# Performance work log

Hardware: AMD Instinct MI355X
Metric: run time of the kernel (lower is better)

## Reference

```python
import jax, jax.numpy as jnp
import numpy as np

B, S, H, NH = 4, 2048, 1024, 16
HD = H // NH  # head dim 64


def setup_inputs() -> dict:
    key = jax.random.key(0)
    ks = jax.random.split(key, 8)
    s = 1.0 / np.sqrt(H)
    return {
        "hidden_states": jax.random.normal(ks[0], (B, S, H), dtype=jnp.float32),
        "attention_mask": jnp.zeros((B, 1, 1, S), dtype=jnp.float32),
        "Wq": jax.random.normal(ks[1], (H, H), dtype=jnp.float32) * s,
        "bq": jnp.zeros((H,), dtype=jnp.float32),
        "Wk": jax.random.normal(ks[2], (H, H), dtype=jnp.float32) * s,
        "bk": jnp.zeros((H,), dtype=jnp.float32),
        "Wv": jax.random.normal(ks[3], (H, H), dtype=jnp.float32) * s,
        "bv": jnp.zeros((H,), dtype=jnp.float32),
    }


def _split_heads(x):
    # [B,S,H] -> [B,NH,S,HD]
    b, s, _ = x.shape
    return x.reshape(b, s, NH, HD).transpose(0, 2, 1, 3)


def reference(hidden_states, attention_mask, Wq, bq, Wk, bk, Wv, bv):
    q = _split_heads(hidden_states @ Wq.T + bq)
    k = _split_heads(hidden_states @ Wk.T + bk)
    v = _split_heads(hidden_states @ Wv.T + bv)

    qk = jnp.einsum("bhid,bhjd->bhij", q, k)  # [B,NH,S,S]
    seq = q.shape[2]
    causal = jnp.triu(jnp.ones((seq, seq), dtype=bool), 1)  # True above diagonal
    attn_w = jnp.where(causal, -jnp.inf, qk) + attention_mask
    # NOTE: original divides by sqrt(d_k) AFTER masking/adding attention_mask
    probs = jax.nn.softmax(attn_w / jnp.sqrt(jnp.float32(HD)), axis=-1)
    out = jnp.einsum("bhij,bhjd->bhid", probs, v)  # [B,NH,S,HD]
    return out.transpose(0, 2, 1, 3).reshape(hidden_states.shape[0], seq, NH * HD)
```

## Files before the change

### kernel.cpp

```cpp
#include <hip/hip_runtime.h>


#define B_   4
#define S_   2048
#define H_   1024
#define NH_  16
#define HD_  64
#define M_   (B_ * S_)

#define CEXP 0.18033688011112042f

#define SWZ(row, col) ((col) ^ (((row) & 7) << 3))

typedef float          f32x4  __attribute__((ext_vector_type(4)));
typedef short          bf16x8 __attribute__((ext_vector_type(8)));
typedef unsigned short u16x8  __attribute__((ext_vector_type(8)));
typedef unsigned int   u32x2  __attribute__((ext_vector_type(2)));

__device__ __forceinline__ unsigned short f2bf(float f) {
    unsigned int u = __float_as_uint(f);
    u += 0x7fffu + ((u >> 16) & 1u);
    return (unsigned short)(u >> 16);
}

__device__ __forceinline__ unsigned int cvt_pk_bf16(float lo, float hi) {
    unsigned int r;
    asm("v_cvt_pk_bf16_f32 %0, %1, %2" : "=v"(r) : "v"(lo), "v"(hi));
    return r;
}

__device__ __forceinline__ void load16_lds(const unsigned short* g, unsigned short* l) {
    __builtin_amdgcn_global_load_lds(
        (const __attribute__((address_space(1))) unsigned int*)g,
        (__attribute__((address_space(3))) unsigned int*)l, 16, 0, 0);
}

__global__ __launch_bounds__(256) void cast_bf16(
    const float* __restrict__ s0, const float* __restrict__ s1,
    const float* __restrict__ s2, const float* __restrict__ s3,
    const float* __restrict__ s4,
    unsigned short* __restrict__ d0, unsigned short* __restrict__ d1,
    unsigned short* __restrict__ d2, unsigned short* __restrict__ d3,
    float* __restrict__ d4) {
    const int bid = blockIdx.x;
    if (bid >= 5632) {
        int i = ((bid - 5632) * 256 + (int)threadIdx.x) * 8;
        if (i + 8 <= B_ * S_) {
            float4 a = *(const float4*)(s4 + i);
            float4 b = *(const float4*)(s4 + i + 4);
            a.x *= CEXP; a.y *= CEXP; a.z *= CEXP; a.w *= CEXP;
            b.x *= CEXP; b.y *= CEXP; b.z *= CEXP; b.w *= CEXP;
            *(float4*)(d4 + i)     = a;
            *(float4*)(d4 + i + 4) = b;
        }
        return;
    }
    const float* src;
    unsigned short* dst;
    int base;
    if (bid < 4096)      { src = s0; dst = d0; base = bid; }
    else if (bid < 4608) { src = s1; dst = d1; base = bid - 4096; }
    else if (bid < 5120) { src = s2; dst = d2; base = bid - 4608; }
    else                 { src = s3; dst = d3; base = bid - 5120; }
    int i = (base * 256 + (int)threadIdx.x) * 8;
    float4 a = *(const float4*)(src + i);
    float4 b = *(const float4*)(src + i + 4);
    u16x8 o;
    o[0] = f2bf(a.x); o[1] = f2bf(a.y); o[2] = f2bf(a.z); o[3] = f2bf(a.w);
    o[4] = f2bf(b.x); o[5] = f2bf(b.y); o[6] = f2bf(b.z); o[7] = f2bf(b.w);
    *(u16x8*)(dst + i) = o;
}

__global__ __launch_bounds__(256, 3) void qkv_gemm(
    const unsigned short* __restrict__ A,
    const unsigned short* __restrict__ W0, const unsigned short* __restrict__ W1,
    const unsigned short* __restrict__ W2,
    const float* __restrict__ b0, const float* __restrict__ b1,
    const float* __restrict__ b2,
    unsigned short* __restrict__ o0, unsigned short* __restrict__ o1,
    unsigned short* __restrict__ o2) {
    __shared__ unsigned short smem[2 * 128 * 64];
    unsigned short* sA = smem;
    unsigned short* sB = smem + 128 * 64;
    unsigned short* sT = smem;

    const int t = threadIdx.x;
    const int w = t >> 6, lane = t & 63, quad = lane >> 4, l15 = lane & 15;
    const int bm = blockIdx.x, bn = blockIdx.y, z = blockIdx.z;

    const unsigned short* W = (z == 0) ? W0 : (z == 1) ? W1 : W2;
    const float*        bia = (z == 0) ? b0 : (z == 1) ? b1 : b2;

    const int wm = (w & 1) * 64, wn = (w >> 1) * 64;

    f32x4 acc[4][4];
#pragma unroll
    for (int i = 0; i < 4; ++i)
#pragma unroll
        for (int j = 0; j < 4; ++j) acc[i][j] = f32x4{0.f, 0.f, 0.f, 0.f};

    const int srow = w * 32 + (lane >> 3);
    const int scol = (lane & 7) * 8;
    const unsigned short* Ag = A + (size_t)(bm * 128 + srow) * H_ + scol;
    const unsigned short* Wg = W + (size_t)(bn * 128 + srow) * H_ + scol;
    unsigned short* lA = &sA[w * 32 * 64];
    unsigned short* lB = &sB[w * 32 * 64];

    for (int kt = 0; kt < 16; ++kt) {
        __syncthreads();
#pragma unroll
        for (int c = 0; c < 4; ++c) {
            load16_lds(Ag + kt * 64 + (size_t)c * 8 * H_, lA + c * 512);
            load16_lds(Wg + kt * 64 + (size_t)c * 8 * H_, lB + c * 512);
        }
        __syncthreads();
#pragma unroll
        for (int kk = 0; kk < 64; kk += 32) {
            bf16x8 af[4], bf[4];
#pragma unroll
            for (int mi = 0; mi < 4; ++mi)
                af[mi] = *(const bf16x8*)&sA[(wm + mi * 16 + l15) * 64 + kk + quad * 8];
#pragma unroll
            for (int ni = 0; ni < 4; ++ni)
                bf[ni] = *(const bf16x8*)&sB[(wn + ni * 16 + l15) * 64 + kk + quad * 8];
#pragma unroll
            for (int mi = 0; mi < 4; ++mi)
#pragma unroll
                for (int ni = 0; ni < 4; ++ni)
                    acc[mi][ni] = __builtin_amdgcn_mfma_f32_16x16x32_bf16(
                        af[mi], bf[ni], acc[mi][ni], 0, 0, 0);
        }
    }

    float bvv[4];
#pragma unroll
    for (int ni = 0; ni < 4; ++ni) bvv[ni] = bia[bn * 128 + wn + ni * 16 + l15];

    if (z != 2) {
        unsigned short* outp = (z == 0) ? o0 : o1;
#pragma unroll
        for (int mi = 0; mi < 4; ++mi)
#pragma unroll
            for (int ni = 0; ni < 4; ++ni)
#pragma unroll
                for (int r = 0; r < 4; ++r) {
                    int m = bm * 128 + wm + mi * 16 + quad * 4 + r;
                    int n = bn * 128 + wn + ni * 16 + l15;
                    outp[(size_t)m * H_ + n] = f2bf(acc[mi][ni][r] + bvv[ni]);
                }
    } else {
        __syncthreads();
        const int halfw = w >> 1;
        const int bb = bm >> 4;
        const int s0 = (bm * 128) & 2047;
        for (int half = 0; half < 2; ++half) {
            if (half) __syncthreads();
            if (halfw == half) {
#pragma unroll
                for (int mi = 0; mi < 4; ++mi)
#pragma unroll
                    for (int ni = 0; ni < 4; ++ni)
#pragma unroll
                        for (int r = 0; r < 4; ++r) {
                            int nl = ni * 16 + l15;
                            int m  = wm + mi * 16 + quad * 4 + r;
                            sT[nl * 136 + m] = f2bf(acc[mi][ni][r] + bvv[ni]);
                        }
            }
            __syncthreads();
            {
                int nl = t >> 2, mc = (t & 3) * 32;
                int ng = bn * 128 + half * 64 + nl;
                int hh = ng >> 6, d = ng & 63;
                size_t base = ((size_t)((bb * NH_ + hh) * HD_ + d)) * S_ + s0 + mc;
#pragma unroll
                for (int i = 0; i < 4; ++i)
                    *(u16x8*)(o2 + base + i * 8) = *(const u16x8*)&sT[nl * 136 + mc + i * 8];
            }
        }
    }
}

__global__ __launch_bounds__(256, 3) void attn(
    const unsigned short* __restrict__ qg, const unsigned short* __restrict__ kg,
    const unsigned short* __restrict__ vtg, const float* __restrict__ mcg,
    float* __restrict__ outg) {
    __shared__ unsigned short k_s[2][64 * 64];
    __shared__ unsigned short v_s[2][64 * 64];
    __shared__ unsigned short p_s[4][16 * 64];

    const int t = threadIdx.x;
    const int w = t >> 6, lane = t & 63, quad = lane >> 4, l15 = lane & 15;
    const int lid = blockIdx.x;
    const int bh = (lid & 7) + ((lid >> 7) << 3);
    const int qt = (lid >> 3) & 15;
    const int b = bh >> 4, h = bh & 15;
    const int qa = qt, qb = 31 - qt;

    const int rs_ = t >> 2;
    const int cs_ = (t & 3) * 16;
    const int sc0 = rs_ * 64 + SWZ(rs_, cs_);
    const int sc1 = rs_ * 64 + SWZ(rs_, cs_ + 8);

    const unsigned short* kbase = kg + ((size_t)b * S_ + rs_) * H_ + h * HD_ + cs_;
    const unsigned short* vbase = vtg + ((size_t)bh * HD_ + rs_) * S_ + cs_;
    const float* mrow = mcg + b * S_ + quad * 4;

    bf16x8 aqa[2], aqb[2];
    {
        const unsigned short* qpa =
            qg + ((size_t)(b * S_ + qa * 64 + w * 16 + l15)) * H_ + h * HD_ + quad * 8;
        aqa[0] = *(const bf16x8*)qpa;
        aqa[1] = *(const bf16x8*)(qpa + 32);
        const unsigned short* qpb =
            qg + ((size_t)(b * S_ + qb * 64 + w * 16 + l15)) * H_ + h * HD_ + quad * 8;
        aqb[0] = *(const bf16x8*)qpb;
        aqb[1] = *(const bf16x8*)(qpb + 32);
    }

    u16x8 pk0 = *(const u16x8*)kbase, pk1 = *(const u16x8*)(kbase + 8);
    u16x8 pv0 = *(const u16x8*)vbase, pv1 = *(const u16x8*)(vbase + 8);

    f32x4 oa[4], ob[4];
    float lsa = 0.f, lsb = 0.f;
#pragma unroll
    for (int dt = 0; dt < 4; ++dt) {
        oa[dt] = f32x4{0.f, 0.f, 0.f, 0.f};
        ob[dt] = f32x4{0.f, 0.f, 0.f, 0.f};
    }

    const int iga0  = qa * 64 + w * 16 + quad * 4;
    const int igb0  = qb * 64 + w * 16 + quad * 4;
    const int qcola = qa * 64 + w * 16 + l15;
    const int qcolb = qb * 64 + w * 16 + l15;
    const int pwr0 = l15 * 64;

    for (int kt = 0; kt <= qb; ++kt) {
        const int cur = kt & 1;
        *(u16x8*)&k_s[cur][sc0] = pk0;
        *(u16x8*)&k_s[cur][sc1] = pk1;
        *(u16x8*)&v_s[cur][sc0] = pv0;
        *(u16x8*)&v_s[cur][sc1] = pv1;
        if (kt < qb) {
            const unsigned short* kp = kbase + (size_t)(kt + 1) * 64 * H_;
            pk0 = *(const u16x8*)kp; pk1 = *(const u16x8*)(kp + 8);
            const unsigned short* vp = vbase + (kt + 1) * 64;
            pv0 = *(const u16x8*)vp; pv1 = *(const u16x8*)(vp + 8);
        }
        __syncthreads();

        float4 mcv[4];
#pragma unroll
        for (int jt = 0; jt < 4; ++jt)
            mcv[jt] = *(const float4*)(mrow + kt * 64 + jt * 16);

        {
            f32x4 sc[4];
#pragma unroll
            for (int jt = 0; jt < 4; ++jt) sc[jt] = f32x4{0.f, 0.f, 0.f, 0.f};
            __builtin_amdgcn_s_setprio(1);
#pragma unroll
            for (int c = 0; c < 2; ++c)
#pragma unroll
                for (int jt = 0; jt < 4; ++jt) {
                    int row = jt * 16 + l15;
                    bf16x8 bk = *(const bf16x8*)&k_s[cur][row * 64 + SWZ(row, c * 32 + quad * 8)];
                    sc[jt] = __builtin_amdgcn_mfma_f32_16x16x32_bf16(bk, aqb[c], sc[jt], 0, 0, 0);
                }
            __builtin_amdgcn_s_setprio(0);
            const bool diag = (kt == qb);
#pragma unroll
            for (int jt = 0; jt < 4; ++jt) {
                const int sb0 = kt * 64 + jt * 16 + quad * 4;
                float p0 = __builtin_amdgcn_exp2f(__builtin_fmaf(sc[jt][0], CEXP, mcv[jt].x));
                float p1 = __builtin_amdgcn_exp2f(__builtin_fmaf(sc[jt][1], CEXP, mcv[jt].y));
                float p2 = __builtin_amdgcn_exp2f(__builtin_fmaf(sc[jt][2], CEXP, mcv[jt].z));
                float p3 = __builtin_amdgcn_exp2f(__builtin_fmaf(sc[jt][3], CEXP, mcv[jt].w));
                if (diag) {
                    if (sb0 + 0 > qcolb) p0 = 0.f;
                    if (sb0 + 1 > qcolb) p1 = 0.f;
                    if (sb0 + 2 > qcolb) p2 = 0.f;
                    if (sb0 + 3 > qcolb) p3 = 0.f;
                }
                lsb += (p0 + p1) + (p2 + p3);
                u32x2 pw;
                pw[0] = cvt_pk_bf16(p0, p1);
                pw[1] = cvt_pk_bf16(p2, p3);
                *(u32x2*)&p_s[w][pwr0 + SWZ(l15, jt * 16 + quad * 4)] = pw;
            }
            __builtin_amdgcn_s_setprio(1);
#pragma unroll
            for (int c = 0; c < 2; ++c) {
                bf16x8 ap = *(const bf16x8*)&p_s[w][l15 * 64 + SWZ(l15, c * 32 + quad * 8)];
#pragma unroll
                for (int dt = 0; dt < 4; ++dt) {
                    int row = dt * 16 + l15;
                    bf16x8 bv = *(const bf16x8*)&v_s[cur][row * 64 + SWZ(row, c * 32 + quad * 8)];
                    ob[dt] = __builtin_amdgcn_mfma_f32_16x16x32_bf16(ap, bv, ob[dt], 0, 0, 0);
                }
            }
            __builtin_amdgcn_s_setprio(0);
        }
        if (kt <= qa) {
            f32x4 sc[4];
#pragma unroll
            for (int jt = 0; jt < 4; ++jt) sc[jt] = f32x4{0.f, 0.f, 0.f, 0.f};
            __builtin_amdgcn_s_setprio(1);
#pragma unroll
            for (int c = 0; c < 2; ++c)
#pragma unroll
                for (int jt = 0; jt < 4; ++jt) {
                    int row = jt * 16 + l15;
                    bf16x8 bk = *(const bf16x8*)&k_s[cur][row * 64 + SWZ(row, c * 32 + quad * 8)];
                    sc[jt] = __builtin_amdgcn_mfma_f32_16x16x32_bf16(bk, aqa[c], sc[jt], 0, 0, 0);
                }
            __builtin_amdgcn_s_setprio(0);
            const bool diag = (kt == qa);
#pragma unroll
            for (int jt = 0; jt < 4; ++jt) {
                const int sb0 = kt * 64 + jt * 16 + quad * 4;
                float p0 = __builtin_amdgcn_exp2f(__builtin_fmaf(sc[jt][0], CEXP, mcv[jt].x));
                float p1 = __builtin_amdgcn_exp2f(__builtin_fmaf(sc[jt][1], CEXP, mcv[jt].y));
                float p2 = __builtin_amdgcn_exp2f(__builtin_fmaf(sc[jt][2], CEXP, mcv[jt].z));
                float p3 = __builtin_amdgcn_exp2f(__builtin_fmaf(sc[jt][3], CEXP, mcv[jt].w));
                if (diag) {
                    if (sb0 + 0 > qcola) p0 = 0.f;
                    if (sb0 + 1 > qcola) p1 = 0.f;
                    if (sb0 + 2 > qcola) p2 = 0.f;
                    if (sb0 + 3 > qcola) p3 = 0.f;
                }
                lsa += (p0 + p1) + (p2 + p3);
                u32x2 pw;
                pw[0] = cvt_pk_bf16(p0, p1);
                pw[1] = cvt_pk_bf16(p2, p3);
                *(u32x2*)&p_s[w][pwr0 + SWZ(l15, jt * 16 + quad * 4)] = pw;
            }
            __builtin_amdgcn_s_setprio(1);
#pragma unroll
            for (int c = 0; c < 2; ++c) {
                bf16x8 ap = *(const bf16x8*)&p_s[w][l15 * 64 + SWZ(l15, c * 32 + quad * 8)];
#pragma unroll
                for (int dt = 0; dt < 4; ++dt) {
                    int row = dt * 16 + l15;
                    bf16x8 bv = *(const bf16x8*)&v_s[cur][row * 64 + SWZ(row, c * 32 + quad * 8)];
                    oa[dt] = __builtin_amdgcn_mfma_f32_16x16x32_bf16(ap, bv, oa[dt], 0, 0, 0);
                }
            }
            __builtin_amdgcn_s_setprio(0);
        }
    }

    float sa = lsa, sb = lsb;
    sa += __shfl_xor(sa, 16); sa += __shfl_xor(sa, 32);
    sb += __shfl_xor(sb, 16); sb += __shfl_xor(sb, 32);
    float ra[4], rb[4];
#pragma unroll
    for (int r = 0; r < 4; ++r) {
        int src = (quad << 4) | (quad * 4 + r);
        ra[r] = 1.0f / __shfl(sa, src);
        rb[r] = 1.0f / __shfl(sb, src);
    }
#pragma unroll
    for (int dt = 0; dt < 4; ++dt)
#pragma unroll
        for (int r = 0; r < 4; ++r) {
            int col = h * HD_ + dt * 16 + l15;
            outg[(size_t)(b * S_ + iga0 + r) * H_ + col] = oa[dt][r] * ra[r];
            outg[(size_t)(b * S_ + igb0 + r) * H_ + col] = ob[dt][r] * rb[r];
        }
}

extern "C" void kernel_launch(void* const* d_in, const int* in_sizes, int n_in,
                              void* d_out, int out_size, void* d_ws, size_t ws_size,
                              hipStream_t stream) {
    const float* hs   = (const float*)d_in[0];
    const float* mask = (const float*)d_in[1];
    const float* Wq   = (const float*)d_in[2];
    const float* bq   = (const float*)d_in[3];
    const float* Wk   = (const float*)d_in[4];
    const float* bk   = (const float*)d_in[5];
    const float* Wv   = (const float*)d_in[6];
    const float* bv   = (const float*)d_in[7];
    float* out = (float*)d_out;

    unsigned short* hsb = (unsigned short*)d_ws;
    unsigned short* wqb = hsb + (size_t)M_ * H_;
    unsigned short* wkb = wqb + (size_t)H_ * H_;
    unsigned short* wvb = wkb + (size_t)H_ * H_;
    unsigned short* qb  = wvb + (size_t)H_ * H_;
    unsigned short* kb  = qb  + (size_t)M_ * H_;
    unsigned short* vtb = kb  + (size_t)M_ * H_;
    float*          mcw = (float*)(vtb + (size_t)M_ * H_);

    cast_bf16<<<dim3(5636), 256, 0, stream>>>(
        hs, Wq, Wk, Wv, mask, hsb, wqb, wkb, wvb, mcw);

    qkv_gemm<<<dim3(M_ / 128, H_ / 128, 3), 256, 0, stream>>>(
        hsb, wqb, wkb, wvb, bq, bk, bv, qb, kb, vtb);

    attn<<<dim3(1024), 256, 0, stream>>>(qb, kb, vtb, mcw, out);
}
```

Baseline: 228.7 us.

## Assign each wave 32 rows of one query tile instead of splitting across both

```diff
diff --git a/kernel.cpp b/kernel.cpp
--- a/kernel.cpp
+++ b/kernel.cpp
@@ -187,7 +187,7 @@
     float* __restrict__ outg) {
     __shared__ unsigned short k_s[2][64 * 64];
     __shared__ unsigned short v_s[2][64 * 64];
-    __shared__ unsigned short p_s[4][16 * 64];
+    __shared__ unsigned short p_s[4][32 * 64];
 
     const int t = threadIdx.x;
     const int w = t >> 6, lane = t & 63, quad = lane >> 4, l15 = lane & 15;
@@ -197,6 +197,11 @@
     const int b = bh >> 4, h = bh & 15;
     const int qa = qt, qb = 31 - qt;
 
+    const bool tile_a = (w >= 2);
+    const int sub = w & 1;
+    const int qtile = tile_a ? qa : qb;
+    const int qbase = qtile * 64 + sub * 32;
+
     const int rs_ = t >> 2;
     const int cs_ = (t & 3) * 16;
     const int sc0 = rs_ * 64 + SWZ(rs_, cs_);
@@ -206,34 +211,30 @@
     const unsigned short* vbase = vtg + ((size_t)bh * HD_ + rs_) * S_ + cs_;
     const float* mrow = mcg + b * S_ + quad * 4;
 
-    bf16x8 aqa[2], aqb[2];
+    bf16x8 aq0[2], aq1[2];
     {
-        const unsigned short* qpa =
-            qg + ((size_t)(b * S_ + qa * 64 + w * 16 + l15)) * H_ + h * HD_ + quad * 8;
-        aqa[0] = *(const bf16x8*)qpa;
-        aqa[1] = *(const bf16x8*)(qpa + 32);
-        const unsigned short* qpb =
-            qg + ((size_t)(b * S_ + qb * 64 + w * 16 + l15)) * H_ + h * HD_ + quad * 8;
-        aqb[0] = *(const bf16x8*)qpb;
-        aqb[1] = *(const bf16x8*)(qpb + 32);
+        const unsigned short* qp0 =
+            qg + ((size_t)(b * S_ + qbase + l15)) * H_ + h * HD_ + quad * 8;
+        aq0[0] = *(const bf16x8*)qp0;
+        aq0[1] = *(const bf16x8*)(qp0 + 32);
+        const unsigned short* qp1 = qp0 + (size_t)16 * H_;
+        aq1[0] = *(const bf16x8*)qp1;
+        aq1[1] = *(const bf16x8*)(qp1 + 32);
     }
 
     u16x8 pk0 = *(const u16x8*)kbase, pk1 = *(const u16x8*)(kbase + 8);
     u16x8 pv0 = *(const u16x8*)vbase, pv1 = *(const u16x8*)(vbase + 8);
 
-    f32x4 oa[4], ob[4];
-    float lsa = 0.f, lsb = 0.f;
+    f32x4 o0[4], o1[4];
+    float ls0 = 0.f, ls1 = 0.f;
 #pragma unroll
     for (int dt = 0; dt < 4; ++dt) {
-        oa[dt] = f32x4{0.f, 0.f, 0.f, 0.f};
-        ob[dt] = f32x4{0.f, 0.f, 0.f, 0.f};
-    }
-
-    const int iga0  = qa * 64 + w * 16 + quad * 4;
-    const int igb0  = qb * 64 + w * 16 + quad * 4;
-    const int qcola = qa * 64 + w * 16 + l15;
-    const int qcolb = qb * 64 + w * 16 + l15;
-    const int pwr0 = l15 * 64;
+        o0[dt] = f32x4{0.f, 0.f, 0.f, 0.f};
+        o1[dt] = f32x4{0.f, 0.f, 0.f, 0.f};
+    }
+
+    const int qcol0 = qbase + l15;
+    const int qcol1 = qbase + 16 + l15;
 
     for (int kt = 0; kt <= qb; ++kt) {
         const int cur = kt & 1;
@@ -249,15 +250,18 @@
         }
         __syncthreads();
 
-        float4 mcv[4];
-#pragma unroll
-        for (int jt = 0; jt < 4; ++jt)
-            mcv[jt] = *(const float4*)(mrow + kt * 64 + jt * 16);
-
-        {
-            f32x4 sc[4];
-#pragma unroll
-            for (int jt = 0; jt < 4; ++jt) sc[jt] = f32x4{0.f, 0.f, 0.f, 0.f};
+        if (!tile_a || kt <= qa) {
+            float4 mcv[4];
+#pragma unroll
+            for (int jt = 0; jt < 4; ++jt)
+                mcv[jt] = *(const float4*)(mrow + kt * 64 + jt * 16);
+
+            f32x4 s0[4], s1[4];
+#pragma unroll
+            for (int jt = 0; jt < 4; ++jt) {
+                s0[jt] = f32x4{0.f, 0.f, 0.f, 0.f};
+                s1[jt] = f32x4{0.f, 0.f, 0.f, 0.f};
+            }
             __builtin_amdgcn_s_setprio(1);
 #pragma unroll
             for (int c = 0; c < 2; ++c)
@@ -265,108 +269,85 @@
                 for (int jt = 0; jt < 4; ++jt) {
                     int row = jt * 16 + l15;
                     bf16x8 bk = *(const bf16x8*)&k_s[cur][row * 64 + SWZ(row, c * 32 + quad * 8)];
-                    sc[jt] = __builtin_amdgcn_mfma_f32_16x16x32_bf16(bk, aqb[c], sc[jt], 0, 0, 0);
+                    s0[jt] = __builtin_amdgcn_mfma_f32_16x16x32_bf16(bk, aq0[c], s0[jt], 0, 0, 0);
+                    s1[jt] = __builtin_amdgcn_mfma_f32_16x16x32_bf16(bk, aq1[c], s1[jt], 0, 0, 0);
                 }
             __builtin_amdgcn_s_setprio(0);
-            const bool diag = (kt == qb);
+
+            const bool diag = (kt == qtile);
 #pragma unroll
             for (int jt = 0; jt < 4; ++jt) {
                 const int sb0 = kt * 64 + jt * 16 + quad * 4;
-                float p0 = __builtin_amdgcn_exp2f(__builtin_fmaf(sc[jt][0], CEXP, mcv[jt].x));
-                float p1 = __builtin_amdgcn_exp2f(__builtin_fmaf(sc[jt][1], CEXP, mcv[jt].y));
-                float p2 = __builtin_amdgcn_exp2f(__builtin_fmaf(sc[jt][2], CEXP, mcv[jt].z));
-                float p3 = __builtin_amdgcn_exp2f(__builtin_fmaf(sc[jt][3], CEXP, mcv[jt].w));
+                float p0 = __builtin_amdgcn_exp2f(__builtin_fmaf(s0[jt][0], CEXP, mcv[jt].x));
+                float p1 = __builtin_amdgcn_exp2f(__builtin_fmaf(s0[jt][1], CEXP, mcv[jt].y));
+                float p2 = __builtin_amdgcn_exp2f(__builtin_fmaf(s0[jt][2], CEXP, mcv[jt].z));
+                float p3 = __builtin_amdgcn_exp2f(__builtin_fmaf(s0[jt][3], CEXP, mcv[jt].w));
                 if (diag) {
-                    if (sb0 + 0 > qcolb) p0 = 0.f;
-                    if (sb0 + 1 > qcolb) p1 = 0.f;
-                    if (sb0 + 2 > qcolb) p2 = 0.f;
-                    if (sb0 + 3 > qcolb) p3 = 0.f;
-                }
-                lsb += (p0 + p1) + (p2 + p3);
+                    if (sb0 + 0 > qcol0) p0 = 0.f;
+                    if (sb0 + 1 > qcol0) p1 = 0.f;
+                    if (sb0 + 2 > qcol0) p2 = 0.f;
+                    if (sb0 + 3 > qcol0) p3 = 0.f;
+                }
+                ls0 += (p0 + p1) + (p2 + p3);
                 u32x2 pw;
                 pw[0] = cvt_pk_bf16(p0, p1);
                 pw[1] = cvt_pk_bf16(p2, p3);
-                *(u32x2*)&p_s[w][pwr0 + SWZ(l15, jt * 16 + quad * 4)] = pw;
-            }
+                *(u32x2*)&p_s[w][l15 * 64 + SWZ(l15, jt * 16 + quad * 4)] = pw;
+            }
+#pragma unroll
+            for (int jt = 0; jt < 4; ++jt) {
+                const int sb0 = kt * 64 + jt * 16 + quad * 4;
+                float p0 = __builtin_amdgcn_exp2f(__builtin_fmaf(s1[jt][0], CEXP, mcv[jt].x));
+                float p1 = __builtin_amdgcn_exp2f(__builtin_fmaf(s1[jt][1], CEXP, mcv[jt].y));
+                float p2 = __builtin_amdgcn_exp2f(__builtin_fmaf(s1[jt][2], CEXP, mcv[jt].z));
+                float p3 = __builtin_amdgcn_exp2f(__builtin_fmaf(s1[jt][3], CEXP, mcv[jt].w));
+                if (diag) {
+                    if (sb0 + 0 > qcol1) p0 = 0.f;
+                    if (sb0 + 1 > qcol1) p1 = 0.f;
+                    if (sb0 + 2 > qcol1) p2 = 0.f;
+                    if (sb0 + 3 > qcol1) p3 = 0.f;
+                }
+                ls1 += (p0 + p1) + (p2 + p3);
+                u32x2 pw;
+                pw[0] = cvt_pk_bf16(p0, p1);
+                pw[1] = cvt_pk_bf16(p2, p3);
+                *(u32x2*)&p_s[w][1024 + l15 * 64 + SWZ(l15, jt * 16 + quad * 4)] = pw;
+            }
+
             __builtin_amdgcn_s_setprio(1);
 #pragma unroll
             for (int c = 0; c < 2; ++c) {
-                bf16x8 ap = *(const bf16x8*)&p_s[w][l15 * 64 + SWZ(l15, c * 32 + quad * 8)];
+                bf16x8 ap0 = *(const bf16x8*)&p_s[w][l15 * 64 + SWZ(l15, c * 32 + quad * 8)];
+                bf16x8 ap1 = *(const bf16x8*)&p_s[w][1024 + l15 * 64 + SWZ(l15, c * 32 + quad * 8)];
 #pragma unroll
                 for (int dt = 0; dt < 4; ++dt) {
                     int row = dt * 16 + l15;
                     bf16x8 bv = *(const bf16x8*)&v_s[cur][row * 64 + SWZ(row, c * 32 + quad * 8)];
-                    ob[dt] = __builtin_amdgcn_mfma_f32_16x16x32_bf16(ap, bv, ob[dt], 0, 0, 0);
+                    o0[dt] = __builtin_amdgcn_mfma_f32_16x16x32_bf16(ap0, bv, o0[dt], 0, 0, 0);
+                    o1[dt] = __builtin_amdgcn_mfma_f32_16x16x32_bf16(ap1, bv, o1[dt], 0, 0, 0);
                 }
             }
             __builtin_amdgcn_s_setprio(0);
         }
-        if (kt <= qa) {
-            f32x4 sc[4];
-#pragma unroll
-            for (int jt = 0; jt < 4; ++jt) sc[jt] = f32x4{0.f, 0.f, 0.f, 0.f};
-            __builtin_amdgcn_s_setprio(1);
-#pragma unroll
-            for (int c = 0; c < 2; ++c)
-#pragma unroll
-                for (int jt = 0; jt < 4; ++jt) {
-                    int row = jt * 16 + l15;
-                    bf16x8 bk = *(const bf16x8*)&k_s[cur][row * 64 + SWZ(row, c * 32 + quad * 8)];
-                    sc[jt] = __builtin_amdgcn_mfma_f32_16x16x32_bf16(bk, aqa[c], sc[jt], 0, 0, 0);
-                }
-            __builtin_amdgcn_s_setprio(0);
-            const bool diag = (kt == qa);
-#pragma unroll
-            for (int jt = 0; jt < 4; ++jt) {
-                const int sb0 = kt * 64 + jt * 16 + quad * 4;
-                float p0 = __builtin_amdgcn_exp2f(__builtin_fmaf(sc[jt][0], CEXP, mcv[jt].x));
-                float p1 = __builtin_amdgcn_exp2f(__builtin_fmaf(sc[jt][1], CEXP, mcv[jt].y));
-                float p2 = __builtin_amdgcn_exp2f(__builtin_fmaf(sc[jt][2], CEXP, mcv[jt].z));
-                float p3 = __builtin_amdgcn_exp2f(__builtin_fmaf(sc[jt][3], CEXP, mcv[jt].w));
-                if (diag) {
-                    if (sb0 + 0 > qcola) p0 = 0.f;
-                    if (sb0 + 1 > qcola) p1 = 0.f;
-                    if (sb0 + 2 > qcola) p2 = 0.f;
-                    if (sb0 + 3 > qcola) p3 = 0.f;
-                }
-                lsa += (p0 + p1) + (p2 + p3);
-                u32x2 pw;
-                pw[0] = cvt_pk_bf16(p0, p1);
-                pw[1] = cvt_pk_bf16(p2, p3);
-                *(u32x2*)&p_s[w][pwr0 + SWZ(l15, jt * 16 + quad * 4)] = pw;
-            }
-            __builtin_amdgcn_s_setprio(1);
-#pragma unroll
-            for (int c = 0; c < 2; ++c) {
-                bf16x8 ap = *(const bf16x8*)&p_s[w][l15 * 64 + SWZ(l15, c * 32 + quad * 8)];
-#pragma unroll
-                for (int dt = 0; dt < 4; ++dt) {
-                    int row = dt * 16 + l15;
-                    bf16x8 bv = *(const bf16x8*)&v_s[cur][row * 64 + SWZ(row, c * 32 + quad * 8)];
-                    oa[dt] = __builtin_amdgcn_mfma_f32_16x16x32_bf16(ap, bv, oa[dt], 0, 0, 0);
-                }
-            }
-            __builtin_amdgcn_s_setprio(0);
-        }
-    }
-
-    float sa = lsa, sb = lsb;
-    sa += __shfl_xor(sa, 16); sa += __shfl_xor(sa, 32);
-    sb += __shfl_xor(sb, 16); sb += __shfl_xor(sb, 32);
-    float ra[4], rb[4];
+    }
+
+    float sA = ls0, sB = ls1;
+    sA += __shfl_xor(sA, 16); sA += __shfl_xor(sA, 32);
+    sB += __shfl_xor(sB, 16); sB += __shfl_xor(sB, 32);
+    float r0[4], r1[4];
 #pragma unroll
     for (int r = 0; r < 4; ++r) {
         int src = (quad << 4) | (quad * 4 + r);
-        ra[r] = 1.0f / __shfl(sa, src);
-        rb[r] = 1.0f / __shfl(sb, src);
+        r0[r] = 1.0f / __shfl(sA, src);
+        r1[r] = 1.0f / __shfl(sB, src);
     }
 #pragma unroll
     for (int dt = 0; dt < 4; ++dt)
 #pragma unroll
         for (int r = 0; r < 4; ++r) {
             int col = h * HD_ + dt * 16 + l15;
-            outg[(size_t)(b * S_ + iga0 + r) * H_ + col] = oa[dt][r] * ra[r];
-            outg[(size_t)(b * S_ + igb0 + r) * H_ + col] = ob[dt][r] * rb[r];
+            outg[(size_t)(b * S_ + qbase + quad * 4 + r) * H_ + col]      = o0[dt][r] * r0[r];
+            outg[(size_t)(b * S_ + qbase + 16 + quad * 4 + r) * H_ + col] = o1[dt][r] * r1[r];
         }
 }
 
```

After: 239.7 us. +4.8%, slower.

## Replace paired causal q-tiles per block with one q-tile per block, heaviest first

Applied to the files above, without the earlier changes.

```diff
diff --git a/kernel.cpp b/kernel.cpp
--- a/kernel.cpp
+++ b/kernel.cpp
@@ -192,10 +192,9 @@
     const int t = threadIdx.x;
     const int w = t >> 6, lane = t & 63, quad = lane >> 4, l15 = lane & 15;
     const int lid = blockIdx.x;
-    const int bh = (lid & 7) + ((lid >> 7) << 3);
-    const int qt = (lid >> 3) & 15;
+    const int bh = (lid & 7) + ((lid >> 8) << 3);
+    const int qt = 31 - ((lid >> 3) & 31);
     const int b = bh >> 4, h = bh & 15;
-    const int qa = qt, qb = 31 - qt;
 
     const int rs_ = t >> 2;
     const int cs_ = (t & 3) * 16;
@@ -206,42 +205,33 @@
     const unsigned short* vbase = vtg + ((size_t)bh * HD_ + rs_) * S_ + cs_;
     const float* mrow = mcg + b * S_ + quad * 4;
 
-    bf16x8 aqa[2], aqb[2];
+    bf16x8 aq[2];
     {
-        const unsigned short* qpa =
-            qg + ((size_t)(b * S_ + qa * 64 + w * 16 + l15)) * H_ + h * HD_ + quad * 8;
-        aqa[0] = *(const bf16x8*)qpa;
-        aqa[1] = *(const bf16x8*)(qpa + 32);
-        const unsigned short* qpb =
-            qg + ((size_t)(b * S_ + qb * 64 + w * 16 + l15)) * H_ + h * HD_ + quad * 8;
-        aqb[0] = *(const bf16x8*)qpb;
-        aqb[1] = *(const bf16x8*)(qpb + 32);
+        const unsigned short* qp =
+            qg + ((size_t)(b * S_ + qt * 64 + w * 16 + l15)) * H_ + h * HD_ + quad * 8;
+        aq[0] = *(const bf16x8*)qp;
+        aq[1] = *(const bf16x8*)(qp + 32);
     }
 
     u16x8 pk0 = *(const u16x8*)kbase, pk1 = *(const u16x8*)(kbase + 8);
     u16x8 pv0 = *(const u16x8*)vbase, pv1 = *(const u16x8*)(vbase + 8);
 
-    f32x4 oa[4], ob[4];
-    float lsa = 0.f, lsb = 0.f;
-#pragma unroll
-    for (int dt = 0; dt < 4; ++dt) {
-        oa[dt] = f32x4{0.f, 0.f, 0.f, 0.f};
-        ob[dt] = f32x4{0.f, 0.f, 0.f, 0.f};
-    }
-
-    const int iga0  = qa * 64 + w * 16 + quad * 4;
-    const int igb0  = qb * 64 + w * 16 + quad * 4;
-    const int qcola = qa * 64 + w * 16 + l15;
-    const int qcolb = qb * 64 + w * 16 + l15;
+    f32x4 o[4];
+    float ls = 0.f;
+#pragma unroll
+    for (int dt = 0; dt < 4; ++dt) o[dt] = f32x4{0.f, 0.f, 0.f, 0.f};
+
+    const int ig0  = qt * 64 + w * 16 + quad * 4;
+    const int qcol = qt * 64 + w * 16 + l15;
     const int pwr0 = l15 * 64;
 
-    for (int kt = 0; kt <= qb; ++kt) {
+    for (int kt = 0; kt <= qt; ++kt) {
         const int cur = kt & 1;
         *(u16x8*)&k_s[cur][sc0] = pk0;
         *(u16x8*)&k_s[cur][sc1] = pk1;
         *(u16x8*)&v_s[cur][sc0] = pv0;
         *(u16x8*)&v_s[cur][sc1] = pv1;
-        if (kt < qb) {
+        if (kt < qt) {
             const unsigned short* kp = kbase + (size_t)(kt + 1) * 64 * H_;
             pk0 = *(const u16x8*)kp; pk1 = *(const u16x8*)(kp + 8);
             const unsigned short* vp = vbase + (kt + 1) * 64;
@@ -254,119 +244,69 @@
         for (int jt = 0; jt < 4; ++jt)
             mcv[jt] = *(const float4*)(mrow + kt * 64 + jt * 16);
 
-        {
-            f32x4 sc[4];
-#pragma unroll
-            for (int jt = 0; jt < 4; ++jt) sc[jt] = f32x4{0.f, 0.f, 0.f, 0.f};
-            __builtin_amdgcn_s_setprio(1);
-#pragma unroll
-            for (int c = 0; c < 2; ++c)
-#pragma unroll
-                for (int jt = 0; jt < 4; ++jt) {
-                    int row = jt * 16 + l15;
-                    bf16x8 bk = *(const bf16x8*)&k_s[cur][row * 64 + SWZ(row, c * 32 + quad * 8)];
-                    sc[jt] = __builtin_amdgcn_mfma_f32_16x16x32_bf16(bk, aqb[c], sc[jt], 0, 0, 0);
-                }
-            __builtin_amdgcn_s_setprio(0);
-            const bool diag = (kt == qb);
+        f32x4 sc[4];
+#pragma unroll
+        for (int jt = 0; jt < 4; ++jt) sc[jt] = f32x4{0.f, 0.f, 0.f, 0.f};
+        __builtin_amdgcn_s_setprio(1);
+#pragma unroll
+        for (int c = 0; c < 2; ++c)
 #pragma unroll
             for (int jt = 0; jt < 4; ++jt) {
-                const int sb0 = kt * 64 + jt * 16 + quad * 4;
-                float p0 = __builtin_amdgcn_exp2f(__builtin_fmaf(sc[jt][0], CEXP, mcv[jt].x));
-                float p1 = __builtin_amdgcn_exp2f(__builtin_fmaf(sc[jt][1], CEXP, mcv[jt].y));
-                float p2 = __builtin_amdgcn_exp2f(__builtin_fmaf(sc[jt][2], CEXP, mcv[jt].z));
-                float p3 = __builtin_amdgcn_exp2f(__builtin_fmaf(sc[jt][3], CEXP, mcv[jt].w));
-                if (diag) {
-                    if (sb0 + 0 > qcolb) p0 = 0.f;
-                    if (sb0 + 1 > qcolb) p1 = 0.f;
-                    if (sb0 + 2 > qcolb) p2 = 0.f;
-                    if (sb0 + 3 > qcolb) p3 = 0.f;
-                }
-                lsb += (p0 + p1) + (p2 + p3);
-                u32x2 pw;
-                pw[0] = cvt_pk_bf16(p0, p1);
-                pw[1] = cvt_pk_bf16(p2, p3);
-                *(u32x2*)&p_s[w][pwr0 + SWZ(l15, jt * 16 + quad * 4)] = pw;
-            }
-            __builtin_amdgcn_s_setprio(1);
-#pragma unroll
-            for (int c = 0; c < 2; ++c) {
-                bf16x8 ap = *(const bf16x8*)&p_s[w][l15 * 64 + SWZ(l15, c * 32 + quad * 8)];
-#pragma unroll
-                for (int dt = 0; dt < 4; ++dt) {
-                    int row = dt * 16 + l15;
-                    bf16x8 bv = *(const bf16x8*)&v_s[cur][row * 64 + SWZ(row, c * 32 + quad * 8)];
-                    ob[dt] = __builtin_amdgcn_mfma_f32_16x16x32_bf16(ap, bv, ob[dt], 0, 0, 0);
-                }
-            }
-            __builtin_amdgcn_s_setprio(0);
-        }
-        if (kt <= qa) {
-            f32x4 sc[4];
-#pragma unroll
-            for (int jt = 0; jt < 4; ++jt) sc[jt] = f32x4{0.f, 0.f, 0.f, 0.f};
-            __builtin_amdgcn_s_setprio(1);
-#pragma unroll
-            for (int c = 0; c < 2; ++c)
-#pragma unroll
-                for (int jt = 0; jt < 4; ++jt) {
-                    int row = jt * 16 + l15;
-                    bf16x8 bk = *(const bf16x8*)&k_s[cur][row * 64 + SWZ(row, c * 32 + quad * 8)];
-                    sc[jt] = __builtin_amdgcn_mfma_f32_16x16x32_bf16(bk, aqa[c], sc[jt], 0, 0, 0);
-                }
-            __builtin_amdgcn_s_setprio(0);
-            const bool diag = (kt == qa);
-#pragma unroll
-            for (int jt = 0; jt < 4; ++jt) {
-                const int sb0 = kt * 64 + jt * 16 + quad * 4;
-                float p0 = __builtin_amdgcn_exp2f(__builtin_fmaf(sc[jt][0], CEXP, mcv[jt].x));
-                float p1 = __builtin_amdgcn_exp2f(__builtin_fmaf(sc[jt][1], CEXP, mcv[jt].y));
-                float p2 = __builtin_amdgcn_exp2f(__builtin_fmaf(sc[jt][2], CEXP, mcv[jt].z));
-                float p3 = __builtin_amdgcn_exp2f(__builtin_fmaf(sc[jt][3], CEXP, mcv[jt].w));
-                if (diag) {
-                    if (sb0 + 0 > qcola) p0 = 0.f;
-                    if (sb0 + 1 > qcola) p1 = 0.f;
-                    if (sb0 + 2 > qcola) p2 = 0.f;
-                    if (sb0 + 3 > qcola) p3 = 0.f;
-                }
-                lsa += (p0 + p1) + (p2 + p3);
-                u32x2 pw;
-                pw[0] = cvt_pk_bf16(p0, p1);
-                pw[1] = cvt_pk_bf16(p2, p3);
-                *(u32x2*)&p_s[w][pwr0 + SWZ(l15, jt * 16 + quad * 4)] = pw;
-            }
-            __builtin_amdgcn_s_setprio(1);
-#pragma unroll
-            for (int c = 0; c < 2; ++c) {
-                bf16x8 ap = *(const bf16x8*)&p_s[w][l15 * 64 + SWZ(l15, c * 32 + quad * 8)];
-#pragma unroll
-                for (int dt = 0; dt < 4; ++dt) {
-                    int row = dt * 16 + l15;
-                    bf16x8 bv = *(const bf16x8*)&v_s[cur][row * 64 + SWZ(row, c * 32 + quad * 8)];
-                    oa[dt] = __builtin_amdgcn_mfma_f32_16x16x32_bf16(ap, bv, oa[dt], 0, 0, 0);
-                }
-            }
-            __builtin_amdgcn_s_setprio(0);
-        }
-    }
-
-    float sa = lsa, sb = lsb;
+                int row = jt * 16 + l15;
+                bf16x8 bk = *(const bf16x8*)&k_s[cur][row * 64 + SWZ(row, c * 32 + quad * 8)];
+                sc[jt] = __builtin_amdgcn_mfma_f32_16x16x32_bf16(bk, aq[c], sc[jt], 0, 0, 0);
+            }
+        __builtin_amdgcn_s_setprio(0);
+
+        const bool diag = (kt == qt);
+#pragma unroll
+        for (int jt = 0; jt < 4; ++jt) {
+            const int sb0 = kt * 64 + jt * 16 + quad * 4;
+            float p0 = __builtin_amdgcn_exp2f(__builtin_fmaf(sc[jt][0], CEXP, mcv[jt].x));
+            float p1 = __builtin_amdgcn_exp2f(__builtin_fmaf(sc[jt][1], CEXP, mcv[jt].y));
+            float p2 = __builtin_amdgcn_exp2f(__builtin_fmaf(sc[jt][2], CEXP, mcv[jt].z));
+            float p3 = __builtin_amdgcn_exp2f(__builtin_fmaf(sc[jt][3], CEXP, mcv[jt].w));
+            if (diag) {
+                if (sb0 + 0 > qcol) p0 = 0.f;
+                if (sb0 + 1 > qcol) p1 = 0.f;
+                if (sb0 + 2 > qcol) p2 = 0.f;
+                if (sb0 + 3 > qcol) p3 = 0.f;
+            }
+            ls += (p0 + p1) + (p2 + p3);
+            u32x2 pw;
+            pw[0] = cvt_pk_bf16(p0, p1);
+            pw[1] = cvt_pk_bf16(p2, p3);
+            *(u32x2*)&p_s[w][pwr0 + SWZ(l15, jt * 16 + quad * 4)] = pw;
+        }
+
+        __builtin_amdgcn_s_setprio(1);
+#pragma unroll
+        for (int c = 0; c < 2; ++c) {
+            bf16x8 ap = *(const bf16x8*)&p_s[w][l15 * 64 + SWZ(l15, c * 32 + quad * 8)];
+#pragma unroll
+            for (int dt = 0; dt < 4; ++dt) {
+                int row = dt * 16 + l15;
+                bf16x8 bv = *(const bf16x8*)&v_s[cur][row * 64 + SWZ(row, c * 32 + quad * 8)];
+                o[dt] = __builtin_amdgcn_mfma_f32_16x16x32_bf16(ap, bv, o[dt], 0, 0, 0);
+            }
+        }
+        __builtin_amdgcn_s_setprio(0);
+    }
+
+    float sa = ls;
     sa += __shfl_xor(sa, 16); sa += __shfl_xor(sa, 32);
-    sb += __shfl_xor(sb, 16); sb += __shfl_xor(sb, 32);
-    float ra[4], rb[4];
+    float ra[4];
 #pragma unroll
     for (int r = 0; r < 4; ++r) {
         int src = (quad << 4) | (quad * 4 + r);
         ra[r] = 1.0f / __shfl(sa, src);
-        rb[r] = 1.0f / __shfl(sb, src);
     }
 #pragma unroll
     for (int dt = 0; dt < 4; ++dt)
 #pragma unroll
         for (int r = 0; r < 4; ++r) {
             int col = h * HD_ + dt * 16 + l15;
-            outg[(size_t)(b * S_ + iga0 + r) * H_ + col] = oa[dt][r] * ra[r];
-            outg[(size_t)(b * S_ + igb0 + r) * H_ + col] = ob[dt][r] * rb[r];
+            outg[(size_t)(b * S_ + ig0 + r) * H_ + col] = o[dt][r] * ra[r];
         }
 }
 
@@ -398,5 +338,5 @@
     qkv_gemm<<<dim3(M_ / 128, H_ / 128, 3), 256, 0, stream>>>(
         hsb, wqb, wkb, wvb, bq, bk, bv, qb, kb, vtb);
 
-    attn<<<dim3(1024), 256, 0, stream>>>(qb, kb, vtb, mcw, out);
-}
+    attn<<<dim3(2048), 256, 0, stream>>>(qb, kb, vtb, mcw, out);
+}
```

After: 224.6 us. Within noise of the previous version (-1.8%).
